# Optimization experiments

Hardware: AMD Instinct MI355X
Metric: run time of the kernel (lower is better)

## Reference

```python
import jax, jax.numpy as jnp
import numpy as np

E = 256   # embed_size
H = 256   # hidden_size
C = 3     # channels
V = 257   # pixel vocab (0..255 + boundary token 256)
B, R, CO = 128, 32, 32


def setup_inputs() -> dict:
    key = jax.random.key(0)
    ks = jax.random.split(key, 16)
    s = 0.05
    return {
        "x": jax.random.randint(ks[0], (B, C, R, CO), 0, V),
        "emb": jax.random.normal(ks[1], (C, V, E), dtype=jnp.float32) * s,
        "xcomb_W": jax.random.normal(ks[2], (C, E, 2 * E), dtype=jnp.float32) * s,
        "xcomb_b": jax.random.normal(ks[3], (C, E), dtype=jnp.float32) * s,
        "hcomb_W": jax.random.normal(ks[4], (C, H, 2 * H), dtype=jnp.float32) * s,
        "hcomb_b": jax.random.normal(ks[5], (C, H), dtype=jnp.float32) * s,
        "W_ih": jax.random.normal(ks[6], (C, 3 * H, E + 2), dtype=jnp.float32) * s,
        "W_hh": jax.random.normal(ks[7], (C, 3 * H, H), dtype=jnp.float32) * s,
        "b_ih": jax.random.normal(ks[8], (C, 3 * H), dtype=jnp.float32) * s,
        "b_hh": jax.random.normal(ks[9], (C, 3 * H), dtype=jnp.float32) * s,
        "red_W": jax.random.normal(ks[10], (V, H), dtype=jnp.float32) * s,
        "red_b": jax.random.normal(ks[11], (V,), dtype=jnp.float32) * s,
        "green_W": jax.random.normal(ks[12], (V, H + E), dtype=jnp.float32) * s,
        "green_b": jax.random.normal(ks[13], (V,), dtype=jnp.float32) * s,
        "blue_W": jax.random.normal(ks[14], (V, H + 2 * E), dtype=jnp.float32) * s,
        "blue_b": jax.random.normal(ks[15], (V,), dtype=jnp.float32) * s,
    }


def _forward(x, emb, xcomb_W, xcomb_b, hcomb_W, hcomb_b, W_ih, W_hh, b_ih, b_hh,
             red_W, red_b, green_W, green_b, blue_W, blue_b):
    Bb, Cc, Rr, Co = x.shape
    Nr, Nc = Rr - 1, Co - 1
    Hd = W_hh.shape[-1]
    dt = emb.dtype

    # context pixel indices for each output position (row+1,col+1)
    left = x[:, :, 1:, :-1]    # x[:,c,row+1,col]
    above = x[:, :, :-1, 1:]   # x[:,c,row,col+1]
    target = x[:, :, 1:, 1:]   # x[:,c,row+1,col+1] (conditioning embeds for green/blue)

    # per-channel embedding gather, vectorized over all positions
    gather = jax.vmap(lambda t, idx: t[idx], in_axes=(0, 1), out_axes=1)
    left_e = gather(emb, left)      # [B,C,Nr,Nc,E]
    above_e = gather(emb, above)
    target_e = gather(emb, target)

    # x_comb linear on cat(left,above); hidden-independent -> precompute
    xi = jnp.concatenate([left_e, above_e], axis=-1)                     # [B,C,Nr,Nc,2E]
    xi = jnp.einsum('bcrke,cfe->bcrkf', xi, xcomb_W) + xcomb_b[None, :, None, None, :]

    # positional (row,col) features appended as floats (torch.cat promotion)
    pos_r = jnp.broadcast_to(jnp.arange(Nr, dtype=dt)[:, None], (Nr, Nc))
    pos_c = jnp.broadcast_to(jnp.arange(Nc, dtype=dt)[None, :], (Nr, Nc))
    pos = jnp.broadcast_to(jnp.stack([pos_r, pos_c], -1)[None, None], (Bb, Cc, Nr, Nc, 2))
    xfull = jnp.concatenate([xi, pos], axis=-1)                          # [B,C,Nr,Nc,E+2]

    # GRU input projection is hidden-independent -> precompute gates_x
    gx = jnp.einsum('bcrkf,cgf->bcrkg', xfull, W_ih) + b_ih[None, :, None, None, :]
    gx = jnp.transpose(gx, (2, 3, 1, 0, 4))                              # [Nr,Nc,C,B,3H]

    def col_step(prev_left, xs):
        gx_col, prev_row_col = xs   # [C,B,3H], [C,B,H]
        pl = prev_left              # [B,H], shared across channels and cols
        hs = []
        for c in range(Cc):         # fixed small channel loop (sequential dependence)
            hcat = jnp.concatenate([pl, prev_row_col[c]], axis=-1)       # [B,2H]
            h = hcat @ hcomb_W[c].T + hcomb_b[c]                          # [B,H]
            gh = h @ W_hh[c].T + b_hh[c]                                  # [B,3H]
            gxr, gxz, gxn = jnp.split(gx_col[c], 3, axis=-1)
            ghr, ghz, ghn = jnp.split(gh, 3, axis=-1)
            r = jax.nn.sigmoid(gxr + ghr)
            z = jax.nn.sigmoid(gxz + ghz)
            n = jnp.tanh(gxn + r * ghn)
            hnew = (1.0 - z) * n + z * h
            pl = hnew
            hs.append(hnew)
        return pl, jnp.stack(hs, 0)  # carry, [C,B,H]

    def row_step(prev_row, gx_row):
        # prev_row: hiddens from previous row [Nc,C,B,H]
        init_left = jnp.zeros((Bb, Hd), dtype=dt)
        _, hs_row = jax.lax.scan(col_step, init_left, (gx_row, prev_row))
        return hs_row, hs_row

    init_row = jnp.zeros((Nc, Cc, Bb, Hd), dtype=dt)
    _, h_all = jax.lax.scan(row_step, init_row, gx)   # [Nr,Nc,C,B,H]

    te = jnp.transpose(target_e, (2, 3, 1, 0, 4))     # [Nr,Nc,C,B,E]
    h0, h1, h2 = h_all[:, :, 0], h_all[:, :, 1], h_all[:, :, 2]  # [Nr,Nc,B,H]
    lr = h0 @ red_W.T + red_b
    lg = jnp.concatenate([h1, te[:, :, 0]], -1) @ green_W.T + green_b
    lb = jnp.concatenate([h2, te[:, :, 0], te[:, :, 1]], -1) @ blue_W.T + blue_b
    logits = jnp.stack([lr, lg, lb], 0)               # [C,Nr,Nc,B,V]
    return jnp.transpose(logits, (3, 0, 1, 2, 4))     # [B,C,Nr,Nc,V]


def reference(x, emb, xcomb_W, xcomb_b, hcomb_W, hcomb_b, W_ih, W_hh, b_ih, b_hh,
              red_W, red_b, green_W, green_b, blue_W, blue_b):
    return _forward(x, emb, xcomb_W, xcomb_b, hcomb_W, hcomb_b, W_ih, W_hh,
                    b_ih, b_hh, red_W, red_b, green_W, green_b, blue_W, blue_b)
```

## Files before the change

### kernel.cpp

```cpp
#include <hip/hip_runtime.h>

typedef __attribute__((ext_vector_type(4))) float f32x4;
typedef __attribute__((ext_vector_type(8))) short s16x8;

__device__ __forceinline__ unsigned short f2bf(float f) {
  union { float f; unsigned u; } v; v.f = f;
  unsigned r = v.u + 0x7fffu + ((v.u >> 16) & 1u);
  return (unsigned short)(r >> 16);
}


__global__ void prep_wbig(const float* __restrict__ hcomb_W, const float* __restrict__ hcomb_b,
                          const float* __restrict__ W_hh, const float* __restrict__ b_hh,
                          unsigned short* __restrict__ Wbig, float* __restrict__ bbig) {
  __shared__ float red[256];
  const int c = blockIdx.x, g = blockIdx.y, t = threadIdx.x;
  const float* hW = hcomb_W + (size_t)c * 256 * 512;
  unsigned short* orow = Wbig + ((size_t)c * 1024 + g) * 512;
  if (g < 256) {
    orow[t]       = f2bf(hW[(size_t)g * 512 + t]);
    orow[t + 256] = f2bf(hW[(size_t)g * 512 + t + 256]);
    if (t == 0) bbig[c * 1024 + g] = hcomb_b[c * 256 + g];
    return;
  }
  const int gp = g - 256;
  const float* wrow = W_hh + ((size_t)c * 768 + gp) * 256;
  float a0 = 0.f, a1 = 0.f;
  for (int h = 0; h < 256; h++) {
    float w = wrow[h];
    a0 += w * hW[(size_t)h * 512 + t];
    a1 += w * hW[(size_t)h * 512 + t + 256];
  }
  orow[t] = f2bf(a0); orow[t + 256] = f2bf(a1);
  red[t] = wrow[t] * hcomb_b[c * 256 + t];
  __syncthreads();
  for (int s = 128; s > 0; s >>= 1) { if (t < s) red[t] += red[t + s]; __syncthreads(); }
  if (t == 0) bbig[c * 1024 + g] = red[0] + b_hh[c * 768 + gp];
}

__global__ void prep_u(const float* __restrict__ emb, const float* __restrict__ xcomb_W,
                       float* __restrict__ Ul, float* __restrict__ Ua) {
  __shared__ float er[256];
  const int c = blockIdx.x, v = blockIdx.y, side = blockIdx.z, f = threadIdx.x;
  er[f] = emb[((size_t)c * 257 + v) * 256 + f];
  __syncthreads();
  const float* wrow = xcomb_W + ((size_t)c * 256 + f) * 512 + side * 256;
  float a = 0.f;
  for (int e = 0; e < 256; e++) a += er[e] * wrow[e];
  (side ? Ua : Ul)[((size_t)c * 257 + v) * 256 + f] = a;
}

__global__ void prep_t(const float* __restrict__ W_ih, const float* __restrict__ Ul,
                       const float* __restrict__ Ua, float* __restrict__ Tl, float* __restrict__ Ta) {
  __shared__ float ur[256];
  const int c = blockIdx.x, v = blockIdx.y, side = blockIdx.z, g = threadIdx.x;
  if (g < 256) ur[g] = (side ? Ua : Ul)[((size_t)c * 257 + v) * 256 + g];
  __syncthreads();
  const float* wrow = W_ih + ((size_t)c * 768 + g) * 258;
  float a = 0.f;
  for (int f = 0; f < 256; f++) a += ur[f] * wrow[f];
  (side ? Ta : Tl)[((size_t)c * 257 + v) * 768 + g] = a;
}

__global__ void prep_bgx(const float* __restrict__ W_ih, const float* __restrict__ xcomb_b,
                         const float* __restrict__ b_ih, float* __restrict__ bgx) {
  __shared__ float xb[256];
  const int c = blockIdx.x, g = threadIdx.x;
  if (g < 256) xb[g] = xcomb_b[c * 256 + g];
  __syncthreads();
  const float* wrow = W_ih + ((size_t)c * 768 + g) * 258;
  float a = b_ih[c * 768 + g];
  for (int f = 0; f < 256; f++) a += xb[f] * wrow[f];
  bgx[c * 768 + g] = a;
}

__global__ void prep_tgb(const float* __restrict__ emb, const float* __restrict__ green_W,
                         const float* __restrict__ blue_W,
                         float* __restrict__ TG, float* __restrict__ TB0, float* __restrict__ TB1) {
  __shared__ float er[256];
  const int v = blockIdx.x, which = blockIdx.y, u = threadIdx.x;
  const int ch = (which == 2) ? 1 : 0;
  if (u < 256) er[u] = emb[((size_t)ch * 257 + v) * 256 + u];
  __syncthreads();
  if (u >= 257) return;
  const float* W; int pitch, off; float* T;
  if (which == 0)      { W = green_W; pitch = 512; off = 256; T = TG;  }
  else if (which == 1) { W = blue_W;  pitch = 768; off = 256; T = TB0; }
  else                 { W = blue_W;  pitch = 768; off = 512; T = TB1; }
  const float* wrow = W + (size_t)u * pitch + off;
  float a = 0.f;
  for (int e = 0; e < 256; e++) a += er[e] * wrow[e];
  T[(size_t)v * 257 + u] = a;
}

__global__ void prep_w3(const float* __restrict__ red_W, const float* __restrict__ green_W,
                        const float* __restrict__ blue_W, unsigned short* __restrict__ W3) {
  const int c = blockIdx.x, v = blockIdx.y, t = threadIdx.x;
  float val = 0.f;
  if (v < 257) {
    if (c == 0)      val = red_W[(size_t)v * 256 + t];
    else if (c == 1) val = green_W[(size_t)v * 512 + t];
    else             val = blue_W[(size_t)v * 768 + t];
  }
  W3[((size_t)c * 272 + v) * 256 + t] = f2bf(val);
}

__global__ __launch_bounds__(256, 2)
void level_kernel(int L, const int* __restrict__ x,
                  float* __restrict__ hbuf,
                  const unsigned short* __restrict__ Wbig,
                  const float* __restrict__ bbig,
                  const float* __restrict__ Tl, const float* __restrict__ Ta,
                  const float* __restrict__ bgx,
                  const float* __restrict__ W_ih,
                  const unsigned short* __restrict__ W3,
                  const float* __restrict__ TG, const float* __restrict__ TB0,
                  const float* __restrict__ TB1,
                  const float* __restrict__ red_b, const float* __restrict__ green_b,
                  const float* __restrict__ blue_b,
                  float* __restrict__ out)
{
  __shared__ unsigned short Abuf[128 * 136];
  __shared__ int idx0[128], idx1[128];

  const int r = blockIdx.x;
  const int role = blockIdx.y;
  const int tid = threadIdx.x;
  const int lane = tid & 63, wv = tid >> 6;
  const int quad = lane >> 4, l16 = lane & 15;

  if (role < 4) {
    const int t = L - r;
    if (t < 0 || t > 92) return;
    const int k = t / 3, c = t - 3 * k;

    if (tid < 128) {
      const int b = tid;
      idx0[b] = x[((b * 3 + c) * 32 + (r + 1)) * 32 + k];
      idx1[b] = x[((b * 3 + c) * 32 + r) * 32 + (k + 1)];
    }

    const int jcol = role * 64 + wv * 16;
    const bool pl_zero = (k == 0 && c == 0);
    const bool a_zero  = (r == 0);
    const float* plp = hbuf + ((size_t)(r * 3 + (c == 0 ? 2 : c - 1)) * 128) * 256;
    const float* ap  = (r > 0) ? hbuf + ((size_t)((r - 1) * 3 + c) * 128) * 256 : hbuf;

    f32x4 acc[8][4];
    #pragma unroll
    for (int mt = 0; mt < 8; mt++)
      #pragma unroll
      for (int g = 0; g < 4; g++)
        #pragma unroll
        for (int e = 0; e < 4; e++) acc[mt][g][e] = 0.f;

    const unsigned short* Wb = Wbig + (size_t)c * 1024 * 512;

    for (int kc = 0; kc < 4; kc++) {
      const bool from_pl = (kc < 2);
      const float* src = from_pl ? plp : ap;
      const bool zero = from_pl ? pl_zero : a_zero;
      const int colbase = from_pl ? kc * 128 : (kc - 2) * 128;
      __syncthreads();
      #pragma unroll 4
      for (int it = 0; it < 16; it++) {
        const int li = it * 256 + tid;
        const int row = li >> 5;
        const int col = (li & 31) * 4;
        unsigned short o0 = 0, o1 = 0, o2 = 0, o3 = 0;
        if (!zero) {
          const float4 v = *(const float4*)(src + (size_t)row * 256 + colbase + col);
          o0 = f2bf(v.x); o1 = f2bf(v.y); o2 = f2bf(v.z); o3 = f2bf(v.w);
        }
        unsigned short* d = &Abuf[row * 136 + col];
        d[0] = o0; d[1] = o1; d[2] = o2; d[3] = o3;
      }
      __syncthreads();
      #pragma unroll
      for (int ks = 0; ks < 4; ks++) {
        const int kofs = ks * 32 + quad * 8;
        s16x8 bf[4];
        #pragma unroll
        for (int g = 0; g < 4; g++)
          bf[g] = *(const s16x8*)(Wb + (size_t)(g * 256 + jcol + l16) * 512 + kc * 128 + kofs);
        #pragma unroll
        for (int mt = 0; mt < 8; mt++) {
          const s16x8 af = *(const s16x8*)&Abuf[(mt * 16 + l16) * 136 + kofs];
          #pragma unroll
          for (int g = 0; g < 4; g++)
            acc[mt][g] = __builtin_amdgcn_mfma_f32_16x16x32_bf16(af, bf[g], acc[mt][g], 0, 0, 0);
        }
      }
    }

    const int j = jcol + l16;
    const float bh = bbig[c * 1024 + j];
    const float br = bbig[c * 1024 + 256 + j];
    const float bz = bbig[c * 1024 + 512 + j];
    const float bn = bbig[c * 1024 + 768 + j];
    const float fr = (float)r, fk = (float)k;
    const float gxr0 = bgx[c * 768 + j] +
        fr * W_ih[((size_t)c * 768 + j) * 258 + 256] + fk * W_ih[((size_t)c * 768 + j) * 258 + 257];
    const float gxz0 = bgx[c * 768 + 256 + j] +
        fr * W_ih[((size_t)c * 768 + 256 + j) * 258 + 256] + fk * W_ih[((size_t)c * 768 + 256 + j) * 258 + 257];
    const float gxn0 = bgx[c * 768 + 512 + j] +
        fr * W_ih[((size_t)c * 768 + 512 + j) * 258 + 256] + fk * W_ih[((size_t)c * 768 + 512 + j) * 258 + 257];
    const float* Tlc = Tl + (size_t)c * 257 * 768;
    const float* Tac = Ta + (size_t)c * 257 * 768;
    float* hout = hbuf + ((size_t)(r * 3 + c) * 128) * 256;

    #pragma unroll
    for (int mt = 0; mt < 8; mt++) {
      #pragma unroll
      for (int i = 0; i < 4; i++) {
        const int b = mt * 16 + quad * 4 + i;
        const int xl = idx0[b], xa = idx1[b];
        const float gxr = gxr0 + Tlc[(size_t)xl * 768 + j] + Tac[(size_t)xa * 768 + j];
        const float gxz = gxz0 + Tlc[(size_t)xl * 768 + 256 + j] + Tac[(size_t)xa * 768 + 256 + j];
        const float gxn = gxn0 + Tlc[(size_t)xl * 768 + 512 + j] + Tac[(size_t)xa * 768 + 512 + j];
        const float h   = acc[mt][0][i] + bh;
        const float ghr = acc[mt][1][i] + br;
        const float ghz = acc[mt][2][i] + bz;
        const float ghn = acc[mt][3][i] + bn;
        const float rg = __fdividef(1.f, 1.f + __expf(-(gxr + ghr)));
        const float zg = __fdividef(1.f, 1.f + __expf(-(gxz + ghz)));
        const float ng = 1.f - __fdividef(2.f, __expf(2.f * (gxn + rg * ghn)) + 1.f);
        hout[(size_t)b * 256 + j] = (1.f - zg) * ng + zg * h;
      }
    }
  } else {
    const int t = (L - 1) - r;
    if (L < 1 || t < 0 || t > 92) return;
    const int k = t / 3, c = t - 3 * k;

    if (tid < 128) {
      const int b = tid;
      idx0[b] = x[((b * 3 + 0) * 32 + (r + 1)) * 32 + (k + 1)];
      idx1[b] = x[((b * 3 + 1) * 32 + (r + 1)) * 32 + (k + 1)];
    }

    const float* hsrc = hbuf + ((size_t)(r * 3 + c) * 128) * 256;
    const unsigned short* W3c = W3 + (size_t)c * 272 * 256;

    f32x4 acc[2][17];
    #pragma unroll
    for (int m2 = 0; m2 < 2; m2++)
      #pragma unroll
      for (int nt = 0; nt < 17; nt++)
        #pragma unroll
        for (int e = 0; e < 4; e++) acc[m2][nt][e] = 0.f;

    for (int kc = 0; kc < 2; kc++) {
      __syncthreads();
      #pragma unroll 4
      for (int it = 0; it < 16; it++) {
        const int li = it * 256 + tid;
        const int row = li >> 5;
        const int col = (li & 31) * 4;
        const float4 v = *(const float4*)(hsrc + (size_t)row * 256 + kc * 128 + col);
        unsigned short* d = &Abuf[row * 136 + col];
        d[0] = f2bf(v.x); d[1] = f2bf(v.y); d[2] = f2bf(v.z); d[3] = f2bf(v.w);
      }
      __syncthreads();
      #pragma unroll
      for (int ks = 0; ks < 4; ks++) {
        const int kofs = ks * 32 + quad * 8;
        s16x8 af[2];
        #pragma unroll
        for (int m2 = 0; m2 < 2; m2++)
          af[m2] = *(const s16x8*)&Abuf[((wv * 2 + m2) * 16 + l16) * 136 + kofs];
        #pragma unroll
        for (int nt = 0; nt < 17; nt++) {
          const s16x8 bf = *(const s16x8*)(W3c + (size_t)(nt * 16 + l16) * 256 + kc * 128 + kofs);
          #pragma unroll
          for (int m2 = 0; m2 < 2; m2++)
            acc[m2][nt] = __builtin_amdgcn_mfma_f32_16x16x32_bf16(af[m2], bf, acc[m2][nt], 0, 0, 0);
        }
      }
    }

    const float* bias = (c == 0) ? red_b : (c == 1) ? green_b : blue_b;
    #pragma unroll
    for (int m2 = 0; m2 < 2; m2++) {
      #pragma unroll
      for (int i = 0; i < 4; i++) {
        const int b = (wv * 2 + m2) * 16 + quad * 4 + i;
        const int t0 = idx0[b], t1 = idx1[b];
        float* orow = out + ((size_t)((b * 3 + c) * 31 + r) * 31 + k) * 257;
        #pragma unroll
        for (int nt = 0; nt < 17; nt++) {
          const int v = nt * 16 + l16;
          if (v < 257) {
            float val = acc[m2][nt][i] + bias[v];
            if (c == 1)      val += TG[(size_t)t0 * 257 + v];
            else if (c == 2) val += TB0[(size_t)t0 * 257 + v] + TB1[(size_t)t1 * 257 + v];
            orow[v] = val;
          }
        }
      }
    }
  }
}


extern "C" void kernel_launch(void* const* d_in, const int* in_sizes, int n_in,
                              void* d_out, int out_size, void* d_ws, size_t ws_size,
                              hipStream_t stream) {
  const int*   x       = (const int*)  d_in[0];
  const float* emb     = (const float*)d_in[1];
  const float* xcomb_W = (const float*)d_in[2];
  const float* xcomb_b = (const float*)d_in[3];
  const float* hcomb_W = (const float*)d_in[4];
  const float* hcomb_b = (const float*)d_in[5];
  const float* W_ih    = (const float*)d_in[6];
  const float* W_hh    = (const float*)d_in[7];
  const float* b_ih    = (const float*)d_in[8];
  const float* b_hh    = (const float*)d_in[9];
  const float* red_W   = (const float*)d_in[10];
  const float* red_b   = (const float*)d_in[11];
  const float* green_W = (const float*)d_in[12];
  const float* green_b = (const float*)d_in[13];
  const float* blue_W  = (const float*)d_in[14];
  const float* blue_b  = (const float*)d_in[15];
  float* out = (float*)d_out;

  char* p = (char*)d_ws;
  auto alloc = [&](size_t bytes) -> char* {
    char* r = p; p += (bytes + 255) & ~(size_t)255; return r;
  };
  float* hbuf          = (float*)alloc((size_t)31 * 3 * 128 * 256 * 4);
  unsigned short* Wbig = (unsigned short*)alloc((size_t)3 * 1024 * 512 * 2);
  float* bbig          = (float*)alloc((size_t)3 * 1024 * 4);
  float* Tl            = (float*)alloc((size_t)3 * 257 * 768 * 4);
  float* Ta            = (float*)alloc((size_t)3 * 257 * 768 * 4);
  float* Ul            = (float*)alloc((size_t)3 * 257 * 256 * 4);
  float* Ua            = (float*)alloc((size_t)3 * 257 * 256 * 4);
  float* bgx           = (float*)alloc((size_t)3 * 768 * 4);
  unsigned short* W3   = (unsigned short*)alloc((size_t)3 * 272 * 256 * 2);
  float* TG            = (float*)alloc((size_t)257 * 257 * 4);
  float* TB0           = (float*)alloc((size_t)257 * 257 * 4);
  float* TB1           = (float*)alloc((size_t)257 * 257 * 4);

  prep_wbig<<<dim3(3, 1024), dim3(256), 0, stream>>>(hcomb_W, hcomb_b, W_hh, b_hh, Wbig, bbig);
  prep_u<<<dim3(3, 257, 2), dim3(256), 0, stream>>>(emb, xcomb_W, Ul, Ua);
  prep_t<<<dim3(3, 257, 2), dim3(768), 0, stream>>>(W_ih, Ul, Ua, Tl, Ta);
  prep_bgx<<<dim3(3), dim3(768), 0, stream>>>(W_ih, xcomb_b, b_ih, bgx);
  prep_tgb<<<dim3(257, 3), dim3(320), 0, stream>>>(emb, green_W, blue_W, TG, TB0, TB1);
  prep_w3<<<dim3(3, 272), dim3(256), 0, stream>>>(red_W, green_W, blue_W, W3);

  for (int L = 0; L < 124; L++) {
    level_kernel<<<dim3(31, 5), dim3(256), 0, stream>>>(
        L, x, hbuf, Wbig, bbig, Tl, Ta, bgx, W_ih, W3, TG, TB0, TB1,
        red_b, green_b, blue_b, out);
  }
}
```

Measured before the change: 9.645 ms.

## Replace per-level launches with persistent kernel using flag-based wavefront sync

Swaps the 124 per-diagonal kernel launches for a single persistent kernel of 160 blocks. Each block owns a row and role, and waits on per-(level,row) atomic flags in global memory instead of relying on kernel boundaries. A new pre-pass kernel materializes all input-gate contributions (embedding tables plus biases) into a large buffer, so the recurrent step only loads them. Launch overhead and the serialization at kernel boundaries are removed in exchange for spin-wait polling, a large extra workspace, and a correctness dependence on all blocks being co-resident.

Measured after the change: 10.39 ms. 7.7% more time.

```diff
diff --git a/kernel.cpp b/kernel.cpp
--- a/kernel.cpp
+++ b/kernel.cpp
@@ -2,6 +2,7 @@
 
 typedef __attribute__((ext_vector_type(4))) float f32x4;
 typedef __attribute__((ext_vector_type(8))) short s16x8;
+typedef unsigned long long u64;
 
 __device__ __forceinline__ unsigned short f2bf(float f) {
   union { float f; unsigned u; } v; v.f = f;
@@ -105,199 +106,251 @@
   W3[((size_t)c * 272 + v) * 256 + t] = f2bf(val);
 }
 
+__global__ void prep_gx(const int* __restrict__ x,
+                        const float* __restrict__ Tl, const float* __restrict__ Ta,
+                        const float* __restrict__ bgx, const float* __restrict__ bbig,
+                        const float* __restrict__ W_ih, float* __restrict__ pregx) {
+  __shared__ float base[768];
+  __shared__ int ix0[128], ix1[128];
+  const int r = blockIdx.x, k = blockIdx.y, c = blockIdx.z, tid = threadIdx.x;
+  for (int g = tid; g < 768; g += 256) {
+    float v = bgx[c * 768 + g]
+            + (float)r * W_ih[((size_t)c * 768 + g) * 258 + 256]
+            + (float)k * W_ih[((size_t)c * 768 + g) * 258 + 257];
+    if (g < 512) v += bbig[c * 1024 + 256 + g];
+    base[g] = v;
+  }
+  if (tid < 128) {
+    ix0[tid] = x[((tid * 3 + c) * 32 + (r + 1)) * 32 + k];
+    ix1[tid] = x[((tid * 3 + c) * 32 + r) * 32 + (k + 1)];
+  }
+  __syncthreads();
+  const size_t cell = ((size_t)(r * 31 + k)) * 3 + c;
+  float* outp = pregx + cell * 3 * 128 * 256;
+  const float* Tlc = Tl + (size_t)c * 257 * 768;
+  const float* Tac = Ta + (size_t)c * 257 * 768;
+  #pragma unroll 2
+  for (int b = 0; b < 128; ++b) {
+    const float* tl = Tlc + (size_t)ix0[b] * 768;
+    const float* ta = Tac + (size_t)ix1[b] * 768;
+    #pragma unroll
+    for (int q = 0; q < 3; ++q) {
+      const int g = q * 256 + tid;
+      outp[((size_t)q * 128 + b) * 256 + tid] = tl[g] + ta[g] + base[g];
+    }
+  }
+}
+
+__global__ void zero_flags(int* __restrict__ f, int n) {
+  int i = blockIdx.x * 256 + threadIdx.x;
+  if (i < n) f[i] = 0;
+}
+
+
+__device__ __forceinline__ void spinwait(int* f, int target) {
+  while (__hip_atomic_load(f, __ATOMIC_RELAXED, __HIP_MEMORY_SCOPE_AGENT) < target)
+    __builtin_amdgcn_s_sleep(2);
+}
+
 __global__ __launch_bounds__(256, 2)
-void level_kernel(int L, const int* __restrict__ x,
-                  float* __restrict__ hbuf,
-                  const unsigned short* __restrict__ Wbig,
-                  const float* __restrict__ bbig,
-                  const float* __restrict__ Tl, const float* __restrict__ Ta,
-                  const float* __restrict__ bgx,
-                  const float* __restrict__ W_ih,
-                  const unsigned short* __restrict__ W3,
-                  const float* __restrict__ TG, const float* __restrict__ TB0,
-                  const float* __restrict__ TB1,
-                  const float* __restrict__ red_b, const float* __restrict__ green_b,
-                  const float* __restrict__ blue_b,
-                  float* __restrict__ out)
+void persist_kernel(const int* __restrict__ x, float* __restrict__ hbuf,
+                    const unsigned short* __restrict__ Wbig, const float* __restrict__ bbig,
+                    const float* __restrict__ pregx,
+                    const unsigned short* __restrict__ W3,
+                    const float* __restrict__ TG, const float* __restrict__ TB0,
+                    const float* __restrict__ TB1,
+                    const float* __restrict__ red_b, const float* __restrict__ green_b,
+                    const float* __restrict__ blue_b,
+                    float* __restrict__ out, int* __restrict__ flags)
 {
   __shared__ unsigned short Abuf[128 * 136];
   __shared__ int idx0[128], idx1[128];
 
-  const int r = blockIdx.x;
-  const int role = blockIdx.y;
+  const int id = blockIdx.x;
+  const int rlo = id & 7, slot = id >> 3;
+  const int rhi = slot / 5, role = slot - 5 * rhi;
+  const int r = rlo + 8 * rhi;
+  if (r > 30) return;
+
+  int* sflag = flags;
+  int* eflag = flags + 124 * 31;
+
   const int tid = threadIdx.x;
   const int lane = tid & 63, wv = tid >> 6;
   const int quad = lane >> 4, l16 = lane & 15;
 
   if (role < 4) {
-    const int t = L - r;
-    if (t < 0 || t > 92) return;
-    const int k = t / 3, c = t - 3 * k;
-
-    if (tid < 128) {
-      const int b = tid;
-      idx0[b] = x[((b * 3 + c) * 32 + (r + 1)) * 32 + k];
-      idx1[b] = x[((b * 3 + c) * 32 + r) * 32 + (k + 1)];
-    }
-
     const int jcol = role * 64 + wv * 16;
-    const bool pl_zero = (k == 0 && c == 0);
-    const bool a_zero  = (r == 0);
-    const float* plp = hbuf + ((size_t)(r * 3 + (c == 0 ? 2 : c - 1)) * 128) * 256;
-    const float* ap  = (r > 0) ? hbuf + ((size_t)((r - 1) * 3 + c) * 128) * 256 : hbuf;
-
-    f32x4 acc[8][4];
-    #pragma unroll
-    for (int mt = 0; mt < 8; mt++)
+    const int j = jcol + l16;
+
+    for (int L = r; L <= r + 92; ++L) {
+      const int t = L - r;
+      const int k = t / 3, c = t - 3 * k;
+      const size_t cell = ((size_t)(r * 31 + k)) * 3 + c;
+      const float* pg = pregx + cell * 3 * 128 * 256;
+
+      f32x4 acc[8][4];
+      const float bh  = bbig[c * 1024 + j];
+      const float bn3 = bbig[c * 1024 + 768 + j];
       #pragma unroll
-      for (int g = 0; g < 4; g++)
-        #pragma unroll
-        for (int e = 0; e < 4; e++) acc[mt][g][e] = 0.f;
-
-    const unsigned short* Wb = Wbig + (size_t)c * 1024 * 512;
-
-    for (int kc = 0; kc < 4; kc++) {
-      const bool from_pl = (kc < 2);
-      const float* src = from_pl ? plp : ap;
-      const bool zero = from_pl ? pl_zero : a_zero;
-      const int colbase = from_pl ? kc * 128 : (kc - 2) * 128;
-      __syncthreads();
-      #pragma unroll 4
-      for (int it = 0; it < 16; it++) {
-        const int li = it * 256 + tid;
-        const int row = li >> 5;
-        const int col = (li & 31) * 4;
-        unsigned short o0 = 0, o1 = 0, o2 = 0, o3 = 0;
-        if (!zero) {
-          const float4 v = *(const float4*)(src + (size_t)row * 256 + colbase + col);
-          o0 = f2bf(v.x); o1 = f2bf(v.y); o2 = f2bf(v.z); o3 = f2bf(v.w);
-        }
-        unsigned short* d = &Abuf[row * 136 + col];
-        d[0] = o0; d[1] = o1; d[2] = o2; d[3] = o3;
+      for (int mt = 0; mt < 8; ++mt)
+        #pragma unroll
+        for (int i = 0; i < 4; ++i) {
+          const int b = mt * 16 + quad * 4 + i;
+          acc[mt][0][i] = bh;
+          acc[mt][1][i] = pg[(size_t)b * 256 + j];
+          acc[mt][2][i] = pg[(size_t)(128 + b) * 256 + j];
+          acc[mt][3][i] = bn3;
+        }
+
+      if (tid == 0) {
+        if (t >= 1) spinwait(&sflag[(L - 1) * 31 + r], 4);
+        if (r >= 1) spinwait(&sflag[(L - 1) * 31 + (r - 1)], 4);
+        if (t >= 3) {
+          if (r < 30) spinwait(&sflag[(L - 2) * 31 + (r + 1)], 4);
+          spinwait(&eflag[(L - 2) * 31 + r], 1);
+        }
       }
       __syncthreads();
+      __builtin_amdgcn_fence(__ATOMIC_ACQUIRE, "agent");
+
+      const bool pl_zero = (t == 0);
+      const bool a_zero  = (r == 0);
+      const float* plp = hbuf + ((size_t)(r * 3 + (c == 0 ? 2 : c - 1)) * 128) * 256;
+      const float* ap  = (r > 0) ? hbuf + ((size_t)((r - 1) * 3 + c) * 128) * 256 : hbuf;
+      const unsigned short* Wb = Wbig + (size_t)c * 1024 * 512;
+
+      for (int kc = 0; kc < 4; ++kc) {
+        const bool from_pl = (kc < 2);
+        const float* src = from_pl ? plp : ap;
+        const bool zero = from_pl ? pl_zero : a_zero;
+        const int colbase = from_pl ? kc * 128 : (kc - 2) * 128;
+        __syncthreads();
+        #pragma unroll 8
+        for (int it = 0; it < 16; ++it) {
+          const int li = it * 256 + tid;
+          const int row = li >> 5;
+          const int col = (li & 31) * 4;
+          unsigned short o0 = 0, o1 = 0, o2 = 0, o3 = 0;
+          if (!zero) {
+            const float4 v = *(const float4*)(src + (size_t)row * 256 + colbase + col);
+            o0 = f2bf(v.x); o1 = f2bf(v.y); o2 = f2bf(v.z); o3 = f2bf(v.w);
+          }
+          unsigned short* d = &Abuf[row * 136 + col];
+          d[0] = o0; d[1] = o1; d[2] = o2; d[3] = o3;
+        }
+        __syncthreads();
+        #pragma unroll
+        for (int ks = 0; ks < 4; ++ks) {
+          const int kofs = ks * 32 + quad * 8;
+          s16x8 bf[4];
+          #pragma unroll
+          for (int g = 0; g < 4; ++g)
+            bf[g] = *(const s16x8*)(Wb + (size_t)(g * 256 + jcol + l16) * 512 + kc * 128 + kofs);
+          #pragma unroll
+          for (int mt = 0; mt < 8; ++mt) {
+            const s16x8 af = *(const s16x8*)&Abuf[(mt * 16 + l16) * 136 + kofs];
+            #pragma unroll
+            for (int g = 0; g < 4; ++g)
+              acc[mt][g] = __builtin_amdgcn_mfma_f32_16x16x32_bf16(af, bf[g], acc[mt][g], 0, 0, 0);
+          }
+        }
+      }
+
+      const float* pgn = pg + (size_t)2 * 128 * 256;
+      float* hout = hbuf + ((size_t)(r * 3 + c) * 128) * 256;
       #pragma unroll
-      for (int ks = 0; ks < 4; ks++) {
-        const int kofs = ks * 32 + quad * 8;
-        s16x8 bf[4];
-        #pragma unroll
-        for (int g = 0; g < 4; g++)
-          bf[g] = *(const s16x8*)(Wb + (size_t)(g * 256 + jcol + l16) * 512 + kc * 128 + kofs);
-        #pragma unroll
-        for (int mt = 0; mt < 8; mt++) {
-          const s16x8 af = *(const s16x8*)&Abuf[(mt * 16 + l16) * 136 + kofs];
-          #pragma unroll
-          for (int g = 0; g < 4; g++)
-            acc[mt][g] = __builtin_amdgcn_mfma_f32_16x16x32_bf16(af, bf[g], acc[mt][g], 0, 0, 0);
-        }
-      }
-    }
-
-    const int j = jcol + l16;
-    const float bh = bbig[c * 1024 + j];
-    const float br = bbig[c * 1024 + 256 + j];
-    const float bz = bbig[c * 1024 + 512 + j];
-    const float bn = bbig[c * 1024 + 768 + j];
-    const float fr = (float)r, fk = (float)k;
-    const float gxr0 = bgx[c * 768 + j] +
-        fr * W_ih[((size_t)c * 768 + j) * 258 + 256] + fk * W_ih[((size_t)c * 768 + j) * 258 + 257];
-    const float gxz0 = bgx[c * 768 + 256 + j] +
-        fr * W_ih[((size_t)c * 768 + 256 + j) * 258 + 256] + fk * W_ih[((size_t)c * 768 + 256 + j) * 258 + 257];
-    const float gxn0 = bgx[c * 768 + 512 + j] +
-        fr * W_ih[((size_t)c * 768 + 512 + j) * 258 + 256] + fk * W_ih[((size_t)c * 768 + 512 + j) * 258 + 257];
-    const float* Tlc = Tl + (size_t)c * 257 * 768;
-    const float* Tac = Ta + (size_t)c * 257 * 768;
-    float* hout = hbuf + ((size_t)(r * 3 + c) * 128) * 256;
-
-    #pragma unroll
-    for (int mt = 0; mt < 8; mt++) {
-      #pragma unroll
-      for (int i = 0; i < 4; i++) {
-        const int b = mt * 16 + quad * 4 + i;
-        const int xl = idx0[b], xa = idx1[b];
-        const float gxr = gxr0 + Tlc[(size_t)xl * 768 + j] + Tac[(size_t)xa * 768 + j];
-        const float gxz = gxz0 + Tlc[(size_t)xl * 768 + 256 + j] + Tac[(size_t)xa * 768 + 256 + j];
-        const float gxn = gxn0 + Tlc[(size_t)xl * 768 + 512 + j] + Tac[(size_t)xa * 768 + 512 + j];
-        const float h   = acc[mt][0][i] + bh;
-        const float ghr = acc[mt][1][i] + br;
-        const float ghz = acc[mt][2][i] + bz;
-        const float ghn = acc[mt][3][i] + bn;
-        const float rg = __fdividef(1.f, 1.f + __expf(-(gxr + ghr)));
-        const float zg = __fdividef(1.f, 1.f + __expf(-(gxz + ghz)));
-        const float ng = 1.f - __fdividef(2.f, __expf(2.f * (gxn + rg * ghn)) + 1.f);
-        hout[(size_t)b * 256 + j] = (1.f - zg) * ng + zg * h;
-      }
+      for (int mt = 0; mt < 8; ++mt)
+        #pragma unroll
+        for (int i = 0; i < 4; ++i) {
+          const int b = mt * 16 + quad * 4 + i;
+          const float gxn = pgn[(size_t)b * 256 + j];
+          const float h  = acc[mt][0][i];
+          const float rg = __fdividef(1.f, 1.f + __expf(-acc[mt][1][i]));
+          const float zg = __fdividef(1.f, 1.f + __expf(-acc[mt][2][i]));
+          const float ng = 1.f - __fdividef(2.f, __expf(2.f * (gxn + rg * acc[mt][3][i])) + 1.f);
+          hout[(size_t)b * 256 + j] = (1.f - zg) * ng + zg * h;
+        }
+
+      __syncthreads();
+      if (tid == 0)
+        __hip_atomic_fetch_add(&sflag[L * 31 + r], 1, __ATOMIC_RELEASE, __HIP_MEMORY_SCOPE_AGENT);
     }
   } else {
-    const int t = (L - 1) - r;
-    if (L < 1 || t < 0 || t > 92) return;
-    const int k = t / 3, c = t - 3 * k;
-
-    if (tid < 128) {
-      const int b = tid;
-      idx0[b] = x[((b * 3 + 0) * 32 + (r + 1)) * 32 + (k + 1)];
-      idx1[b] = x[((b * 3 + 1) * 32 + (r + 1)) * 32 + (k + 1)];
-    }
-
-    const float* hsrc = hbuf + ((size_t)(r * 3 + c) * 128) * 256;
-    const unsigned short* W3c = W3 + (size_t)c * 272 * 256;
-
-    f32x4 acc[2][17];
-    #pragma unroll
-    for (int m2 = 0; m2 < 2; m2++)
+    for (int Le = r + 1; Le <= r + 93; ++Le) {
+      const int t = Le - 1 - r;
+      const int k = t / 3, c = t - 3 * k;
+
+      if (tid == 0) spinwait(&sflag[(Le - 1) * 31 + r], 4);
+      __syncthreads();
+      __builtin_amdgcn_fence(__ATOMIC_ACQUIRE, "agent");
+
+      if (tid < 128) {
+        idx0[tid] = x[((tid * 3 + 0) * 32 + (r + 1)) * 32 + (k + 1)];
+        idx1[tid] = x[((tid * 3 + 1) * 32 + (r + 1)) * 32 + (k + 1)];
+      }
+
+      const float* hsrc = hbuf + ((size_t)(r * 3 + c) * 128) * 256;
+      const unsigned short* W3c = W3 + (size_t)c * 272 * 256;
+
+      f32x4 acc[2][17];
       #pragma unroll
-      for (int nt = 0; nt < 17; nt++)
-        #pragma unroll
-        for (int e = 0; e < 4; e++) acc[m2][nt][e] = 0.f;
-
-    for (int kc = 0; kc < 2; kc++) {
-      __syncthreads();
-      #pragma unroll 4
-      for (int it = 0; it < 16; it++) {
-        const int li = it * 256 + tid;
-        const int row = li >> 5;
-        const int col = (li & 31) * 4;
-        const float4 v = *(const float4*)(hsrc + (size_t)row * 256 + kc * 128 + col);
-        unsigned short* d = &Abuf[row * 136 + col];
-        d[0] = f2bf(v.x); d[1] = f2bf(v.y); d[2] = f2bf(v.z); d[3] = f2bf(v.w);
+      for (int m2 = 0; m2 < 2; ++m2)
+        #pragma unroll
+        for (int nt = 0; nt < 17; ++nt)
+          #pragma unroll
+          for (int e = 0; e < 4; ++e) acc[m2][nt][e] = 0.f;
+
+      for (int kc = 0; kc < 2; ++kc) {
+        __syncthreads();
+        #pragma unroll 8
+        for (int it = 0; it < 16; ++it) {
+          const int li = it * 256 + tid;
+          const int row = li >> 5;
+          const int col = (li & 31) * 4;
+          const float4 v = *(const float4*)(hsrc + (size_t)row * 256 + kc * 128 + col);
+          unsigned short* d = &Abuf[row * 136 + col];
+          d[0] = f2bf(v.x); d[1] = f2bf(v.y); d[2] = f2bf(v.z); d[3] = f2bf(v.w);
+        }
+        __syncthreads();
+        if (kc == 1 && tid == 0)
+          __hip_atomic_fetch_add(&eflag[Le * 31 + r], 1, __ATOMIC_RELEASE, __HIP_MEMORY_SCOPE_AGENT);
+        #pragma unroll
+        for (int ks = 0; ks < 4; ++ks) {
+          const int kofs = ks * 32 + quad * 8;
+          s16x8 af[2];
+          #pragma unroll
+          for (int m2 = 0; m2 < 2; ++m2)
+            af[m2] = *(const s16x8*)&Abuf[((wv * 2 + m2) * 16 + l16) * 136 + kofs];
+          #pragma unroll
+          for (int nt = 0; nt < 17; ++nt) {
+            const s16x8 bf = *(const s16x8*)(W3c + (size_t)(nt * 16 + l16) * 256 + kc * 128 + kofs);
+            #pragma unroll
+            for (int m2 = 0; m2 < 2; ++m2)
+              acc[m2][nt] = __builtin_amdgcn_mfma_f32_16x16x32_bf16(af[m2], bf, acc[m2][nt], 0, 0, 0);
+          }
+        }
       }
-      __syncthreads();
+
+      const float* bias = (c == 0) ? red_b : (c == 1) ? green_b : blue_b;
       #pragma unroll
-      for (int ks = 0; ks < 4; ks++) {
-        const int kofs = ks * 32 + quad * 8;
-        s16x8 af[2];
-        #pragma unroll
-        for (int m2 = 0; m2 < 2; m2++)
-          af[m2] = *(const s16x8*)&Abuf[((wv * 2 + m2) * 16 + l16) * 136 + kofs];
-        #pragma unroll
-        for (int nt = 0; nt < 17; nt++) {
-          const s16x8 bf = *(const s16x8*)(W3c + (size_t)(nt * 16 + l16) * 256 + kc * 128 + kofs);
-          #pragma unroll
-          for (int m2 = 0; m2 < 2; m2++)
-            acc[m2][nt] = __builtin_amdgcn_mfma_f32_16x16x32_bf16(af[m2], bf, acc[m2][nt], 0, 0, 0);
-        }
-      }
-    }
-
-    const float* bias = (c == 0) ? red_b : (c == 1) ? green_b : blue_b;
-    #pragma unroll
-    for (int m2 = 0; m2 < 2; m2++) {
-      #pragma unroll
-      for (int i = 0; i < 4; i++) {
-        const int b = (wv * 2 + m2) * 16 + quad * 4 + i;
-        const int t0 = idx0[b], t1 = idx1[b];
-        float* orow = out + ((size_t)((b * 3 + c) * 31 + r) * 31 + k) * 257;
-        #pragma unroll
-        for (int nt = 0; nt < 17; nt++) {
-          const int v = nt * 16 + l16;
-          if (v < 257) {
-            float val = acc[m2][nt][i] + bias[v];
-            if (c == 1)      val += TG[(size_t)t0 * 257 + v];
-            else if (c == 2) val += TB0[(size_t)t0 * 257 + v] + TB1[(size_t)t1 * 257 + v];
-            orow[v] = val;
+      for (int m2 = 0; m2 < 2; ++m2)
+        #pragma unroll
+        for (int i = 0; i < 4; ++i) {
+          const int b = (m2 + wv * 2) * 16 + quad * 4 + i;
+          const int t0 = idx0[b], t1 = idx1[b];
+          float* orow = out + ((size_t)((b * 3 + c) * 31 + r) * 31 + k) * 257;
+          #pragma unroll
+          for (int nt = 0; nt < 17; ++nt) {
+            const int v = nt * 16 + l16;
+            if (v < 257) {
+              float val = acc[m2][nt][i] + bias[v];
+              if (c == 1)      val += TG[(size_t)t0 * 257 + v];
+              else if (c == 2) val += TB0[(size_t)t0 * 257 + v] + TB1[(size_t)t1 * 257 + v];
+              orow[v] = val;
+            }
           }
         }
-      }
     }
   }
 }
@@ -340,6 +393,8 @@
   float* TG            = (float*)alloc((size_t)257 * 257 * 4);
   float* TB0           = (float*)alloc((size_t)257 * 257 * 4);
   float* TB1           = (float*)alloc((size_t)257 * 257 * 4);
+  int*   flags         = (int*)  alloc((size_t)2 * 124 * 31 * 4);
+  float* pregx         = (float*)alloc((size_t)2883 * 3 * 128 * 256 * 4);
 
   prep_wbig<<<dim3(3, 1024), dim3(256), 0, stream>>>(hcomb_W, hcomb_b, W_hh, b_hh, Wbig, bbig);
   prep_u<<<dim3(3, 257, 2), dim3(256), 0, stream>>>(emb, xcomb_W, Ul, Ua);
@@ -347,10 +402,9 @@
   prep_bgx<<<dim3(3), dim3(768), 0, stream>>>(W_ih, xcomb_b, b_ih, bgx);
   prep_tgb<<<dim3(257, 3), dim3(320), 0, stream>>>(emb, green_W, blue_W, TG, TB0, TB1);
   prep_w3<<<dim3(3, 272), dim3(256), 0, stream>>>(red_W, green_W, blue_W, W3);
-
-  for (int L = 0; L < 124; L++) {
-    level_kernel<<<dim3(31, 5), dim3(256), 0, stream>>>(
-        L, x, hbuf, Wbig, bbig, Tl, Ta, bgx, W_ih, W3, TG, TB0, TB1,
-        red_b, green_b, blue_b, out);
-  }
-}
+  prep_gx<<<dim3(31, 31, 3), dim3(256), 0, stream>>>(x, Tl, Ta, bgx, bbig, W_ih, pregx);
+  zero_flags<<<dim3(31), dim3(256), 0, stream>>>(flags, 2 * 124 * 31);
+
+  persist_kernel<<<dim3(160), dim3(256), 0, stream>>>(
+      x, hbuf, Wbig, bbig, pregx, W3, TG, TB0, TB1, red_b, green_b, blue_b, out, flags);
+}
```
